# Optimization experiments

Measured on AMD Instinct MI355X. Metric: run time of the kernel, lower is better.

Reference implementation:

```python
import jax, jax.numpy as jnp
import numpy as np
import math

KAPPA = 80.0
N_REJ = 64  # fixed rounds of vectorized rejection sampling (accept prob > 0.5 per round)


def _log_iv(v, x, terms=500):
    # log of modified Bessel I_v(x) via series, in log-space for stability
    ks = np.arange(terms)
    lg1 = np.array([math.lgamma(k + 1.0) for k in range(terms)])
    lg2 = np.array([math.lgamma(v + k + 1.0) for k in range(terms)])
    logt = (v + 2.0 * ks) * np.log(x / 2.0) - lg1 - lg2
    m = logt.max()
    return m + np.log(np.exp(logt - m).sum())


def _vmf_kld(k, d):
    # matches VMF._vmf_kld: k*iv(d/2+1,k)/iv(d/2,k) + d/2*ln k - ln iv(d/2,k) - lgamma(d/2+1) - d/2*ln 2
    ratio = np.exp(_log_iv(d / 2.0 + 1.0, k) - _log_iv(d / 2.0, k))
    return (k * ratio + d / 2.0 * np.log(k) - _log_iv(d / 2.0, k)
            - math.lgamma(d / 2.0 + 1.0) - d / 2.0 * np.log(2.0))


def setup_inputs() -> dict:
    B, H, D = 16384, 1024, 512
    key = jax.random.key(0)
    k1, k2 = jax.random.split(key)
    input_repr = jax.random.normal(k1, (B, H), jnp.float32)
    W = jax.random.normal(k2, (H, D), jnp.float32) * 0.02
    b = jnp.zeros((D,), jnp.float32)
    kld = jnp.array([_vmf_kld(KAPPA, D)], jnp.float32)
    return {"input_repr": input_repr, "W": W, "b": b, "kld": kld, "n_sample": 1}


def _sample_w(key, kappa, D, batch):
    # Wood's rejection sampler for the vMF radial component, batched + masked
    dim = float(D - 1)
    bb = dim / (np.sqrt(4.0 * kappa ** 2 + dim ** 2) + 2.0 * kappa)
    xx = (1.0 - bb) / (1.0 + bb)
    cc = kappa * xx + dim * np.log(1.0 - xx ** 2)
    kz, ku = jax.random.split(key)
    z = jax.random.beta(kz, dim / 2.0, dim / 2.0, (N_REJ, batch))  # [R,B]
    u = jax.random.uniform(ku, (N_REJ, batch))
    w = (1.0 - (1.0 + bb) * z) / (1.0 - (1.0 - bb) * z)
    accept = kappa * w + dim * jnp.log(1.0 - xx * w) - cc >= jnp.log(u)
    idx = jnp.argmax(accept, axis=0)  # first accepted proposal per sample
    return w[idx, jnp.arange(batch)]  # [B]


def reference(input_repr, W, b, kld, n_sample):
    B = input_repr.shape[0]
    D = W.shape[1]
    # estimate_param: FeedForward(softplus) then L2-normalize
    mu_raw = jax.nn.softplus(input_repr @ W + b)          # [B,D]
    norm = jnp.linalg.norm(mu_raw, axis=1, keepdims=True)  # [B,1]
    redundant_norm = (norm - 1.0) ** 2                     # [B,1]
    mu = mu_raw / norm
    # sample_cell (n_sample == 1 path)
    key = jax.random.key(42)
    kw, kv = jax.random.split(key)
    w = _sample_w(kw, KAPPA, D, B)[:, None]                # [B,1]
    v = jax.random.normal(kv, (B, D), mu.dtype)
    proj = jnp.sum(mu * v, axis=1, keepdims=True)
    ortho = v - mu * proj
    v_hat = ortho / jnp.linalg.norm(ortho, axis=1, keepdims=True)
    sampled = v_hat * jnp.sqrt(1.0 - w ** 2) + mu * w      # [B,D]
    return mu, redundant_norm, kld, sampled[None]          # sampled: [1,B,D]
```

## Files before the change

kernel.cpp:

```cpp
#include <hip/hip_runtime.h>
#include <cstdint>
#include <cmath>

struct U2 { uint32_t a, b; };

__host__ __device__ inline uint32_t rotl32(uint32_t v, int r) {
    return (v << r) | (v >> (32 - r));
}

__host__ __device__ inline U2 tf2x32(U2 k, uint32_t x0, uint32_t x1) {
    uint32_t ks0 = k.a, ks1 = k.b, ks2 = k.a ^ k.b ^ 0x1BD11BDAu;
    x0 += ks0; x1 += ks1;
#define TF_R(r) { x0 += x1; x1 = rotl32(x1, r); x1 ^= x0; }
    TF_R(13) TF_R(15) TF_R(26) TF_R(6)
    x0 += ks1; x1 += ks2 + 1u;
    TF_R(17) TF_R(29) TF_R(16) TF_R(24)
    x0 += ks2; x1 += ks0 + 2u;
    TF_R(13) TF_R(15) TF_R(26) TF_R(6)
    x0 += ks0; x1 += ks1 + 3u;
    TF_R(17) TF_R(29) TF_R(16) TF_R(24)
    x0 += ks1; x1 += ks2 + 4u;
    TF_R(13) TF_R(15) TF_R(26) TF_R(6)
    x0 += ks2; x1 += ks0 + 5u;
#undef TF_R
    U2 r; r.a = x0; r.b = x1; return r;
}

__device__ inline float bits_to_u01(uint32_t bits) {
    return __uint_as_float((bits >> 9) | 0x3f800000u) - 1.0f;
}

__device__ inline float erfinv_xla(float x) {
    #pragma clang fp contract(off)
    float w = -log1pf(-(x * x));
    float p;
    if (w < 5.0f) {
        w = w - 2.5f;
        p = 2.81022636e-08f;
        p = 3.43273939e-07f + p * w;
        p = -3.5233877e-06f + p * w;
        p = -4.39150654e-06f + p * w;
        p = 0.00021858087f + p * w;
        p = -0.00125372503f + p * w;
        p = -0.00417768164f + p * w;
        p = 0.246640727f + p * w;
        p = 1.50140941f + p * w;
    } else {
        w = sqrtf(w) - 3.0f;
        p = -0.000200214257f;
        p = 0.000100950558f + p * w;
        p = 0.00134934322f + p * w;
        p = -0.00367342844f + p * w;
        p = 0.00573950773f + p * w;
        p = -0.0076224613f + p * w;
        p = 0.00943887047f + p * w;
        p = 1.00167406f + p * w;
        p = 2.83297682f + p * w;
    }
    return p * x;
}

__device__ inline float bits_to_normal(uint32_t bits) {
    #pragma clang fp contract(off)
    float f = bits_to_u01(bits);
    const float lo = -0.99999994f;
    float u = f * 2.0f + lo;
    u = fmaxf(lo, u);
    return 1.4142135623730951f * erfinv_xla(u);
}

__device__ inline float bits_to_normal_fast(uint32_t bits) {
    float f = bits_to_u01(bits);
    const float lo = -0.99999994f;
    float x = fmaxf(lo, fmaf(f, 2.0f, lo));
    float w = -__logf(fmaf(-x, x, 1.0f));
    float p;
    if (w < 5.0f) {
        w = w - 2.5f;
        p = 2.81022636e-08f;
        p = fmaf(p, w, 3.43273939e-07f);
        p = fmaf(p, w, -3.5233877e-06f);
        p = fmaf(p, w, -4.39150654e-06f);
        p = fmaf(p, w, 0.00021858087f);
        p = fmaf(p, w, -0.00125372503f);
        p = fmaf(p, w, -0.00417768164f);
        p = fmaf(p, w, 0.246640727f);
        p = fmaf(p, w, 1.50140941f);
    } else {
        w = sqrtf(w) - 3.0f;
        p = -0.000200214257f;
        p = fmaf(p, w, 0.000100950558f);
        p = fmaf(p, w, 0.00134934322f);
        p = fmaf(p, w, -0.00367342844f);
        p = fmaf(p, w, 0.00573950773f);
        p = fmaf(p, w, -0.0076224613f);
        p = fmaf(p, w, 0.00943887047f);
        p = fmaf(p, w, 1.00167406f);
        p = fmaf(p, w, 2.83297682f);
    }
    return 1.4142135623730951f * (p * x);
}

__device__ inline float normal_scalar(U2 key) {
    return bits_to_normal(tf2x32(key, 0u, 0u).a);
}

__device__ inline float uniform_scalar(U2 key) {
    uint32_t bits = tf2x32(key, 0u, 0u).a;
    return bits_to_u01(bits);
}

__device__ float gamma_log_one(U2 key, float d, float c) {
    #pragma clang fp contract(off)
    float X = 0.0f, V = 1.0f, U = 2.0f;
    for (;;) {
        float x2 = X * X;
        float sq = 1.0f - 0.0331f * (x2 * x2);
        bool cont;
        if (U < sq) {
            cont = false;
        } else {
            float rhs = X * (0.5f * X) + d * ((1.0f - V) + logf(V));
            cont = (logf(U) >= rhs);
        }
        if (!cont) break;

        U2 t03 = tf2x32(key, 0u, 3u);
        U2 t14 = tf2x32(key, 1u, 4u);
        U2 t25 = tf2x32(key, 2u, 5u);
        U2 nkey; nkey.a = t03.a; nkey.b = t14.a;
        U2 xkey; xkey.a = t25.a; xkey.b = t03.b;
        U2 Ukey; Ukey.a = t14.b; Ukey.b = t25.b;
        key = nkey;

        float x, v;
        do {
            U2 s02 = tf2x32(xkey, 0u, 2u);
            U2 s13 = tf2x32(xkey, 1u, 3u);
            U2 sub; sub.a = s02.b; sub.b = s13.b;
            xkey.a = s02.a; xkey.b = s13.a;
            x = normal_scalar(sub);
            v = 1.0f + c * x;
        } while (v <= 0.0f);
        X = x;
        V = (v * v) * v;
        U = uniform_scalar(Ukey);
    }
    return logf(d) + logf(V);
}

__device__ inline unsigned short f2bf(float f) {
    uint32_t u = __float_as_uint(f);
    uint32_t r = (u + 0x7FFFu + ((u >> 16) & 1u)) >> 16;
    return (unsigned short)r;
}

__device__ inline uint32_t pkbf2(float a, float b) {
    return (uint32_t)f2bf(a) | ((uint32_t)f2bf(b) << 16);
}

__device__ void wood_w_par(int e, U2 key_a, U2 key_b, U2 ku, float xxf,
                           float ccf, float Ap, float Bm, float d, float c,
                           float* __restrict__ w_out) {
    #pragma clang fp contract(off)
    const int lane = threadIdx.x & 63;
    const int s = lane & 3;
    const int gbase = lane & ~3;
    float w0 = 0.0f, w_sel = 0.0f;
    bool done = false;
    for (int base = 0; base < 64 && !done; base += 4) {
        const int r = base + s;
        uint32_t j = (uint32_t)r * 16384u + (uint32_t)e;
        uint32_t m0 = 2u * j, m1 = 2u * j + 1u;
        U2 ka, kb;
        if (m1 < 1048576u) {
            ka.a = tf2x32(key_a, m0, m0 + 1048576u).a;
            ka.b = tf2x32(key_a, m1, m1 + 1048576u).a;
            kb.a = tf2x32(key_b, m0, m0 + 1048576u).a;
            kb.b = tf2x32(key_b, m1, m1 + 1048576u).a;
        } else {
            ka.a = tf2x32(key_a, m0 - 1048576u, m0).b;
            ka.b = tf2x32(key_a, m1 - 1048576u, m1).b;
            kb.a = tf2x32(key_b, m0 - 1048576u, m0).b;
            kb.b = tf2x32(key_b, m1 - 1048576u, m1).b;
        }
        float lga = gamma_log_one(ka, d, c);
        float lgb = gamma_log_one(kb, d, c);
        float mx = fmaxf(lga, lgb);
        float ga = expf(lga - mx), gb = expf(lgb - mx);
        float z = ga / (ga + gb);
        uint32_t ub = (j < 524288u) ? tf2x32(ku, j, j + 524288u).a
                                    : tf2x32(ku, j - 524288u, j).b;
        float u = bits_to_u01(ub);
        float w = (1.0f - Ap * z) / (1.0f - Bm * z);
        float lhs = (80.0f * w + 511.0f * logf(1.0f - xxf * w)) - ccf;
        bool acc = lhs >= logf(u);
        if (base == 0) w0 = __shfl(w, gbase, 64);
        unsigned long long m = __ballot(acc);
        unsigned nib = (unsigned)((m >> gbase) & 0xFull);
        if (nib) {
            int first = __ffs((int)nib) - 1;
            w_sel = __shfl(w, gbase + first, 64);
            done = true;
        }
    }
    if (!done) w_sel = w0;
    if (s == 0) w_out[e] = w_sel;
}

__global__ __launch_bounds__(256) void prep3(
    const float* __restrict__ A, unsigned short* __restrict__ Ab,
    const float* __restrict__ Wm, unsigned short* __restrict__ Wt,
    const float* __restrict__ kld, float* __restrict__ kldo,
    U2 key_a, U2 key_b, U2 ku, float xxf, float ccf, float Ap, float Bm,
    float d, float c, float* __restrict__ wbuf) {
    __shared__ float t[64][65];
    const int b = blockIdx.x;
    if (b < 256) {
        const int wavid = threadIdx.x >> 6;
        const int e = b * 64 + wavid * 16 + ((threadIdx.x & 63) >> 2);
        wood_w_par(e, key_a, key_b, ku, xxf, ccf, Ap, Bm, d, c, wbuf);
    } else if (b < 4352) {
        const int row = (b - 256) * 4 + (threadIdx.x >> 6);
        const int lane = threadIdx.x & 63;
        const float* src = A + (size_t)row * 1024;
        unsigned short* dst = Ab + (size_t)row * 1024;
        const int rx = row & 7;
        #pragma unroll
        for (int q = 0; q < 4; ++q) {
            const int k0 = q * 256 + lane * 4;
            float4 v = *(const float4*)(src + k0);
            ushort4 w;
            w.x = f2bf(v.x); w.y = f2bf(v.y); w.z = f2bf(v.z); w.w = f2bf(v.w);
            const int kt = k0 >> 6;
            const int g = (k0 >> 3) & 7;
            const int e2 = k0 & 7;
            *(ushort4*)(dst + kt * 64 + ((g ^ rx) << 3) + e2) = w;
        }
    } else if (b < 4480) {
        const int tb = b - 4352;
        const int kb = tb & 15;
        const int nb = tb >> 4;
        const int tx = threadIdx.x & 63;
        const int ty = threadIdx.x >> 6;
        #pragma unroll
        for (int i = 0; i < 64; i += 4)
            t[i + ty][tx] = Wm[(size_t)(kb * 64 + i + ty) * 512 + nb * 64 + tx];
        __syncthreads();
        const int g = tx >> 3, e2 = tx & 7;
        #pragma unroll
        for (int i = 0; i < 64; i += 4) {
            int n = i + ty;
            int nglob = nb * 64 + n;
            int p = g ^ (nglob & 7);
            Wt[(size_t)nglob * 1024 + kb * 64 + p * 8 + e2] = f2bf(t[tx][n]);
        }
    } else {
        if (threadIdx.x == 0) kldo[0] = kld[0];
    }
}

typedef __attribute__((ext_vector_type(8))) short bf16x8;
typedef __attribute__((ext_vector_type(4))) float f32x4;

__device__ inline void gll16(const void* g, void* l) {
    __builtin_amdgcn_global_load_lds(
        (const __attribute__((address_space(1))) void*)g,
        (__attribute__((address_space(3))) void*)l, 16, 0, 0);
}

__global__ __launch_bounds__(256) void gemm_dma(
    const unsigned short* __restrict__ Ab, const unsigned short* __restrict__ Wt,
    const float* __restrict__ bias, float* __restrict__ out) {
    __shared__ __align__(16) unsigned short Asm[2][8192];
    __shared__ __align__(16) unsigned short Bsm[2][8192];
    const int tid = threadIdx.x;
    const int b = blockIdx.x;
    const int swz = (b & 7) * 64 + (b >> 3);
    const int bm = swz >> 2;
    const int bn = swz & 3;
    const int wave = tid >> 6, lane = tid & 63;
    const int wm = wave >> 1, wn = wave & 1;
    const int lr = lane & 15, lg = lane >> 4;

    f32x4 acc[4][4] = {};

    const char* aBase = (const char*)Ab +
        (size_t)(bm * 128 + wave * 32 + (lane >> 3)) * 2048 + (lane & 7) * 16;
    const char* bBase = (const char*)Wt +
        (size_t)(bn * 128 + wave * 32 + (lane >> 3)) * 2048 + (lane & 7) * 16;

#define STAGE(ktv, buf)                                                     \
    {                                                                       \
        _Pragma("unroll")                                                   \
        for (int ii = 0; ii < 4; ++ii) {                                    \
            const int chunk = wave * 4 + ii;                                \
            gll16(aBase + (size_t)ii * 8 * 2048 + (ktv) * 128,              \
                  (void*)&Asm[buf][chunk * 512]);                           \
            gll16(bBase + (size_t)ii * 8 * 2048 + (ktv) * 128,              \
                  (void*)&Bsm[buf][chunk * 512]);                           \
        }                                                                   \
    }

    STAGE(0, 0);
    STAGE(1, 1);
    asm volatile("s_waitcnt vmcnt(8)" ::: "memory");
    __builtin_amdgcn_s_barrier();
    __builtin_amdgcn_sched_barrier(0);

    int cur = 0;
    for (int kt = 0; kt < 16; ++kt) {
        #pragma unroll
        for (int ks = 0; ks < 2; ++ks) {
            bf16x8 af[4], bfr[4];
            #pragma unroll
            for (int mi = 0; mi < 4; ++mi) {
                const int r = wm * 64 + mi * 16 + lr;
                const int p = (ks * 4 + lg) ^ (r & 7);
                af[mi] = *(const bf16x8*)&Asm[cur][r * 64 + p * 8];
            }
            #pragma unroll
            for (int ni = 0; ni < 4; ++ni) {
                const int r = wn * 64 + ni * 16 + lr;
                const int p = (ks * 4 + lg) ^ (r & 7);
                bfr[ni] = *(const bf16x8*)&Bsm[cur][r * 64 + p * 8];
            }
            #pragma unroll
            for (int mi = 0; mi < 4; ++mi)
                #pragma unroll
                for (int ni = 0; ni < 4; ++ni)
                    acc[mi][ni] = __builtin_amdgcn_mfma_f32_16x16x32_bf16(
                        af[mi], bfr[ni], acc[mi][ni], 0, 0, 0);
        }
        __builtin_amdgcn_sched_barrier(0);
        __builtin_amdgcn_s_barrier();
        if (kt + 2 < 16) {
            STAGE(kt + 2, cur);
            asm volatile("s_waitcnt vmcnt(8)" ::: "memory");
        } else {
            asm volatile("s_waitcnt vmcnt(0)" ::: "memory");
        }
        __builtin_amdgcn_s_barrier();
        __builtin_amdgcn_sched_barrier(0);
        cur ^= 1;
    }
#undef STAGE

    #pragma unroll
    for (int mi = 0; mi < 4; ++mi) {
        #pragma unroll
        for (int ni = 0; ni < 4; ++ni) {
            const int col = bn * 128 + wn * 64 + ni * 16 + lr;
            const float bcol = bias[col];
            #pragma unroll
            for (int r = 0; r < 4; ++r) {
                const int row = bm * 128 + wm * 64 + mi * 16 + lg * 4 + r;
                float x = acc[mi][ni][r] + bcol;
                float sp = fmaxf(x, 0.0f) + __logf(1.0f + __expf(-fabsf(x)));
                out[(size_t)row * 512 + col] = sp;
            }
        }
    }
}

__device__ void wood_w_one(int i, U2 key_a, U2 key_b, U2 ku, float xxf,
                           float ccf, float Ap, float Bm, float d, float c,
                           float* __restrict__ w_out) {
    #pragma clang fp contract(off)
    float w_sel = 0.0f, w0 = 0.0f;
    bool found = false;
    for (int r = 0; r < 64 && !found; ++r) {
        uint32_t j = (uint32_t)r * 16384u + (uint32_t)i;
        uint32_t m0 = 2u * j, m1 = 2u * j + 1u;
        U2 ka, kb;
        if (m1 < 1048576u) {
            ka.a = tf2x32(key_a, m0, m0 + 1048576u).a;
            ka.b = tf2x32(key_a, m1, m1 + 1048576u).a;
            kb.a = tf2x32(key_b, m0, m0 + 1048576u).a;
            kb.b = tf2x32(key_b, m1, m1 + 1048576u).a;
        } else {
            ka.a = tf2x32(key_a, m0 - 1048576u, m0).b;
            ka.b = tf2x32(key_a, m1 - 1048576u, m1).b;
            kb.a = tf2x32(key_b, m0 - 1048576u, m0).b;
            kb.b = tf2x32(key_b, m1 - 1048576u, m1).b;
        }
        float lga = gamma_log_one(ka, d, c);
        float lgb = gamma_log_one(kb, d, c);
        float mx = fmaxf(lga, lgb);
        float ga = expf(lga - mx), gb = expf(lgb - mx);
        float z = ga / (ga + gb);
        uint32_t ub = (j < 524288u) ? tf2x32(ku, j, j + 524288u).a
                                    : tf2x32(ku, j - 524288u, j).b;
        float u = bits_to_u01(ub);
        float w = (1.0f - Ap * z) / (1.0f - Bm * z);
        float lhs = (80.0f * w + 511.0f * logf(1.0f - xxf * w)) - ccf;
        bool acc = lhs >= logf(u);
        if (r == 0) w0 = w;
        if (acc) { w_sel = w; found = true; }
    }
    w_out[i] = found ? w_sel : w0;
}

__global__ __launch_bounds__(256) void transpose_w(
    const float* __restrict__ Wm, unsigned short* __restrict__ Wt) {
    __shared__ float t[64][65];
    const int kb = blockIdx.x;
    const int nb = blockIdx.y;
    const int tx = threadIdx.x & 63;
    const int ty = threadIdx.x >> 6;
    #pragma unroll
    for (int i = 0; i < 64; i += 4)
        t[i + ty][tx] = Wm[(size_t)(kb * 64 + i + ty) * 512 + nb * 64 + tx];
    __syncthreads();
    const int g = tx >> 3, e = tx & 7;
    #pragma unroll
    for (int i = 0; i < 64; i += 4) {
        int n = i + ty;
        int nglob = nb * 64 + n;
        int p = g ^ (nglob & 7);
        Wt[(size_t)nglob * 1024 + kb * 64 + p * 8 + e] = f2bf(t[tx][n]);
    }
}

__global__ __launch_bounds__(256) void gemm_bf16(
    const float* __restrict__ A, const unsigned short* __restrict__ Wt,
    const float* __restrict__ bias, float* __restrict__ out) {
    __shared__ __align__(16) unsigned short Asm[128 * 64];
    __shared__ __align__(16) unsigned short Bsm[128 * 64];
    const int tid = threadIdx.x;
    const int b = blockIdx.x;
    const int swz = (b & 7) * 64 + (b >> 3);
    const int bm = swz >> 2;
    const int bn = swz & 3;
    const int wave = tid >> 6, lane = tid & 63;
    const int wm = wave >> 1, wn = wave & 1;
    const int lr = lane & 15, lg = lane >> 4;

    f32x4 acc[4][4] = {};

    const int ar = tid >> 1;
    const int ah = tid & 1;
    const float* Ap = A + (size_t)(bm * 128 + ar) * 1024 + ah * 32;
    const int arx = ar & 7;

    const char* WtB = (const char*)Wt;
    const int brow = bn * 128 + (wave * 4) * 8 + (lane >> 3);
    const int bposb = (lane & 7) * 16;

    for (int kt = 0; kt < 16; ++kt) {
        #pragma unroll
        for (int ii = 0; ii < 4; ++ii) {
            const int chunk = wave * 4 + ii;
            const void* src = WtB + (size_t)(brow + ii * 8) * 2048 + kt * 128 + bposb;
            gll16(src, (void*)&Bsm[chunk * 512]);
        }
        const float* srcA = Ap + kt * 64;
        #pragma unroll
        for (int st = 0; st < 4; ++st) {
            float4 y0 = *(const float4*)(srcA + st * 8);
            float4 y1 = *(const float4*)(srcA + st * 8 + 4);
            uint4 uv;
            uv.x = pkbf2(y0.x, y0.y);
            uv.y = pkbf2(y0.z, y0.w);
            uv.z = pkbf2(y1.x, y1.y);
            uv.w = pkbf2(y1.z, y1.w);
            const int gblk = ah * 4 + st;
            const int p = gblk ^ arx;
            *(uint4*)&Asm[ar * 64 + p * 8] = uv;
        }
        __syncthreads();

        #pragma unroll
        for (int ks = 0; ks < 2; ++ks) {
            bf16x8 af[4], bfr[4];
            #pragma unroll
            for (int mi = 0; mi < 4; ++mi) {
                const int r = wm * 64 + mi * 16 + lr;
                const int p = (ks * 4 + lg) ^ (r & 7);
                af[mi] = *(const bf16x8*)&Asm[r * 64 + p * 8];
            }
            #pragma unroll
            for (int ni = 0; ni < 4; ++ni) {
                const int r = wn * 64 + ni * 16 + lr;
                const int p = (ks * 4 + lg) ^ (r & 7);
                bfr[ni] = *(const bf16x8*)&Bsm[r * 64 + p * 8];
            }
            #pragma unroll
            for (int mi = 0; mi < 4; ++mi)
                #pragma unroll
                for (int ni = 0; ni < 4; ++ni)
                    acc[mi][ni] = __builtin_amdgcn_mfma_f32_16x16x32_bf16(
                        af[mi], bfr[ni], acc[mi][ni], 0, 0, 0);
        }
        __syncthreads();
    }

    #pragma unroll
    for (int mi = 0; mi < 4; ++mi) {
        #pragma unroll
        for (int ni = 0; ni < 4; ++ni) {
            const int col = bn * 128 + wn * 64 + ni * 16 + lr;
            const float bcol = bias[col];
            #pragma unroll
            for (int r = 0; r < 4; ++r) {
                const int row = bm * 128 + wm * 64 + mi * 16 + lg * 4 + r;
                float x = acc[mi][ni][r] + bcol;
                float sp = fmaxf(x, 0.0f) + log1pf(expf(-fabsf(x)));
                out[(size_t)row * 512 + col] = sp;
            }
        }
    }
}

__global__ __launch_bounds__(64) void compute_w_kernel(
    U2 key_a, U2 key_b, U2 ku, float xxf, float ccf, float Ap, float Bm,
    float d, float c, float* __restrict__ w_out) {
    const int i = blockIdx.x * blockDim.x + threadIdx.x;
    if (i >= 16384) return;
    wood_w_one(i, key_a, key_b, ku, xxf, ccf, Ap, Bm, d, c, w_out);
}

__global__ void copy_kld(const float* __restrict__ kld, float* __restrict__ dst) {
    if (blockIdx.x == 0 && threadIdx.x == 0) dst[0] = kld[0];
}

__device__ inline float wave_allreduce(float s) {
    #pragma unroll
    for (int off = 1; off < 64; off <<= 1) s += __shfl_xor(s, off);
    return s;
}

__global__ __launch_bounds__(256) void finalize2(
    const float* muraw, float* muout, float* __restrict__ rn,
    const float* __restrict__ wv, U2 kv, float* smp) {
    const int p = blockIdx.x * 4 + (threadIdx.x >> 6);
    const int lane = threadIdx.x & 63;
    const int r0 = p, r1 = p + 8192;
    const float* q0 = muraw + (size_t)r0 * 512;
    const float* q1 = muraw + (size_t)r1 * 512;

    float m0[8], m1[8];
    {
        float4 t0 = *(const float4*)(q0 + lane * 4);
        float4 t1 = *(const float4*)(q0 + 256 + lane * 4);
        m0[0] = t0.x; m0[1] = t0.y; m0[2] = t0.z; m0[3] = t0.w;
        m0[4] = t1.x; m0[5] = t1.y; m0[6] = t1.z; m0[7] = t1.w;
        float4 t2 = *(const float4*)(q1 + lane * 4);
        float4 t3 = *(const float4*)(q1 + 256 + lane * 4);
        m1[0] = t2.x; m1[1] = t2.y; m1[2] = t2.z; m1[3] = t2.w;
        m1[4] = t3.x; m1[5] = t3.y; m1[6] = t3.z; m1[7] = t3.w;
    }

    float ss0 = 0.0f, ss1 = 0.0f;
    #pragma unroll
    for (int j = 0; j < 8; ++j) { ss0 += m0[j] * m0[j]; ss1 += m1[j] * m1[j]; }
    float n0 = sqrtf(wave_allreduce(ss0));
    float n1 = sqrtf(wave_allreduce(ss1));
    if (lane == 0) {
        float d0 = n0 - 1.0f, d1 = n1 - 1.0f;
        rn[r0] = d0 * d0;
        rn[r1] = d1 * d1;
    }
    float in0 = 1.0f / n0, in1 = 1.0f / n1;
    #pragma unroll
    for (int j = 0; j < 8; ++j) { m0[j] *= in0; m1[j] *= in1; }

    float v0[8], v1[8];
    #pragma unroll
    for (int j = 0; j < 8; ++j) {
        const int c = (j < 4) ? (lane * 4 + j) : (256 + lane * 4 + (j - 4));
        uint32_t idx = (uint32_t)p * 512u + (uint32_t)c;
        U2 h = tf2x32(kv, idx, idx + 4194304u);
        v0[j] = bits_to_normal_fast(h.a);
        v1[j] = bits_to_normal_fast(h.b);
    }

    float p0 = 0.0f, p1 = 0.0f;
    #pragma unroll
    for (int j = 0; j < 8; ++j) { p0 += m0[j] * v0[j]; p1 += m1[j] * v1[j]; }
    p0 = wave_allreduce(p0);
    p1 = wave_allreduce(p1);

    float o0[8], o1[8];
    float s0 = 0.0f, s1 = 0.0f;
    #pragma unroll
    for (int j = 0; j < 8; ++j) {
        o0[j] = v0[j] - m0[j] * p0; s0 += o0[j] * o0[j];
        o1[j] = v1[j] - m1[j] * p1; s1 += o1[j] * o1[j];
    }
    float f0, f1, w0, w1;
    {
        float on0 = sqrtf(wave_allreduce(s0));
        float on1 = sqrtf(wave_allreduce(s1));
        w0 = wv[r0]; w1 = wv[r1];
        f0 = sqrtf(1.0f - w0 * w0) / on0;
        f1 = sqrtf(1.0f - w1 * w1) / on1;
    }

    float* pm0 = muout + (size_t)r0 * 512;
    float* pm1 = muout + (size_t)r1 * 512;
    float* op0 = smp + (size_t)r0 * 512;
    float* op1 = smp + (size_t)r1 * 512;
    float4 wvec;
    wvec.x = o0[0] * f0 + m0[0] * w0; wvec.y = o0[1] * f0 + m0[1] * w0;
    wvec.z = o0[2] * f0 + m0[2] * w0; wvec.w = o0[3] * f0 + m0[3] * w0;
    *(float4*)(op0 + lane * 4) = wvec;
    wvec.x = o0[4] * f0 + m0[4] * w0; wvec.y = o0[5] * f0 + m0[5] * w0;
    wvec.z = o0[6] * f0 + m0[6] * w0; wvec.w = o0[7] * f0 + m0[7] * w0;
    *(float4*)(op0 + 256 + lane * 4) = wvec;
    wvec.x = o1[0] * f1 + m1[0] * w1; wvec.y = o1[1] * f1 + m1[1] * w1;
    wvec.z = o1[2] * f1 + m1[2] * w1; wvec.w = o1[3] * f1 + m1[3] * w1;
    *(float4*)(op1 + lane * 4) = wvec;
    wvec.x = o1[4] * f1 + m1[4] * w1; wvec.y = o1[5] * f1 + m1[5] * w1;
    wvec.z = o1[6] * f1 + m1[6] * w1; wvec.w = o1[7] * f1 + m1[7] * w1;
    *(float4*)(op1 + 256 + lane * 4) = wvec;

    wvec.x = m0[0]; wvec.y = m0[1]; wvec.z = m0[2]; wvec.w = m0[3];
    *(float4*)(pm0 + lane * 4) = wvec;
    wvec.x = m0[4]; wvec.y = m0[5]; wvec.z = m0[6]; wvec.w = m0[7];
    *(float4*)(pm0 + 256 + lane * 4) = wvec;
    wvec.x = m1[0]; wvec.y = m1[1]; wvec.z = m1[2]; wvec.w = m1[3];
    *(float4*)(pm1 + lane * 4) = wvec;
    wvec.x = m1[4]; wvec.y = m1[5]; wvec.z = m1[6]; wvec.w = m1[7];
    *(float4*)(pm1 + 256 + lane * 4) = wvec;
}

extern "C" void kernel_launch(void* const* d_in, const int* in_sizes, int n_in,
                              void* d_out, int out_size, void* d_ws, size_t ws_size,
                              hipStream_t stream) {
    const float* A    = (const float*)d_in[0];
    const float* Wm   = (const float*)d_in[1];
    const float* bias = (const float*)d_in[2];
    const float* kld  = (const float*)d_in[3];

    float* out = (float*)d_out;
    float* mu   = out;
    float* rn   = out + 8388608;
    float* kldo = out + 8388608 + 16384;
    float* smp  = kldo + 1;
    float* wbuf = (float*)d_ws;

    U2 root; root.a = 0u; root.b = 42u;
    U2 t02 = tf2x32(root, 0u, 2u), t13 = tf2x32(root, 1u, 3u);
    U2 kw; kw.a = t02.a; kw.b = t13.a;
    U2 kv; kv.a = t02.b; kv.b = t13.b;
    U2 s02 = tf2x32(kw, 0u, 2u), s13 = tf2x32(kw, 1u, 3u);
    U2 kz; kz.a = s02.a; kz.b = s13.a;
    U2 ku; ku.a = s02.b; ku.b = s13.b;
    U2 b02 = tf2x32(kz, 0u, 2u), b13 = tf2x32(kz, 1u, 3u);
    U2 key_a; key_a.a = b02.a; key_a.b = b13.a;
    U2 key_b; key_b.a = b02.b; key_b.b = b13.b;

    const double kappa = 80.0, dim = 511.0;
    double bb = dim / (sqrt(4.0 * kappa * kappa + dim * dim) + 2.0 * kappa);
    double xxd = (1.0 - bb) / (1.0 + bb);
    double ccd = kappa * xxd + dim * log(1.0 - xxd * xxd);
    float xxf = (float)xxd, ccf = (float)ccd;
    float Apc = (float)(1.0 + bb), Bmc = (float)(1.0 - bb);
    float one3 = 1.0f / 3.0f;
    float dml = 255.5f - one3;
    float cml = one3 / sqrtf(dml);

    const bool bigws = ws_size >= (size_t)(65536 + 1048576);
    if (bigws) {
        unsigned short* Ab = (unsigned short*)d_out;
        unsigned short* Wt = (unsigned short*)((char*)d_ws + 65536);
        float* muraw = smp;
        prep3<<<4481, 256, 0, stream>>>(A, Ab, Wm, Wt, kld, kldo,
                                        key_a, key_b, ku, xxf, ccf, Apc, Bmc,
                                        dml, cml, wbuf);
        gemm_dma<<<512, 256, 0, stream>>>(Ab, Wt, bias, muraw);
        finalize2<<<2048, 256, 0, stream>>>(muraw, mu, rn, wbuf, kv, smp);
    } else {
        unsigned short* Wt = (unsigned short*)((char*)d_out + 33619984);
        compute_w_kernel<<<256, 64, 0, stream>>>(key_a, key_b, ku, xxf, ccf,
                                                 Apc, Bmc, dml, cml, wbuf);
        transpose_w<<<dim3(16, 8), 256, 0, stream>>>(Wm, Wt);
        gemm_bf16<<<512, 256, 0, stream>>>(A, Wt, bias, mu);
        finalize2<<<2048, 256, 0, stream>>>(mu, mu, rn, wbuf, kv, smp);
        copy_kld<<<1, 64, 0, stream>>>(kld, kldo);
    }
}
```

Before: 69.75 us.

## Fuse GEMM with normalize and vMF sampling epilogue in one kernel

Replaces the 128x128-tile GEMM plus separate finalize kernel with a single kernel where each 512-thread block computes full 512-column rows for 32 rows (two 16-row groups), then does softplus, L2 norm, random normal generation, projection and sampling in the epilogue using cross-wave shared-memory reductions. The bf16 staging layout changes to 32-wide K tiles with a 4-way swizzle. This removes the round trip of the raw mu matrix through global memory and one kernel launch. In exchange, the A-operand tile is small, so the whole W matrix is re-read from L2 by every block, and the epilogue adds several block barriers.

```diff
diff --git a/kernel.cpp b/kernel.cpp
--- a/kernel.cpp
+++ b/kernel.cpp
@@ -208,7 +208,7 @@
     if (s == 0) w_out[e] = w_sel;
 }
 
-__global__ __launch_bounds__(256) void prep3(
+__global__ __launch_bounds__(256) void prep4(
     const float* __restrict__ A, unsigned short* __restrict__ Ab,
     const float* __restrict__ Wm, unsigned short* __restrict__ Wt,
     const float* __restrict__ kld, float* __restrict__ kldo,
@@ -225,17 +225,17 @@
         const int lane = threadIdx.x & 63;
         const float* src = A + (size_t)row * 1024;
         unsigned short* dst = Ab + (size_t)row * 1024;
-        const int rx = row & 7;
+        const int rx = (row >> 1) & 3;
         #pragma unroll
         for (int q = 0; q < 4; ++q) {
             const int k0 = q * 256 + lane * 4;
             float4 v = *(const float4*)(src + k0);
             ushort4 w;
             w.x = f2bf(v.x); w.y = f2bf(v.y); w.z = f2bf(v.z); w.w = f2bf(v.w);
-            const int kt = k0 >> 6;
-            const int g = (k0 >> 3) & 7;
+            const int kt = k0 >> 5;
+            const int g = (k0 >> 3) & 3;
             const int e2 = k0 & 7;
-            *(ushort4*)(dst + kt * 64 + ((g ^ rx) << 3) + e2) = w;
+            *(ushort4*)(dst + kt * 32 + ((g ^ rx) << 3) + e2) = w;
         }
     } else if (b < 4480) {
         const int tb = b - 4352;
@@ -247,13 +247,15 @@
         for (int i = 0; i < 64; i += 4)
             t[i + ty][tx] = Wm[(size_t)(kb * 64 + i + ty) * 512 + nb * 64 + tx];
         __syncthreads();
-        const int g = tx >> 3, e2 = tx & 7;
+        const int kt = (tx >> 5);
+        const int g = (tx >> 3) & 3;
+        const int e2 = tx & 7;
         #pragma unroll
         for (int i = 0; i < 64; i += 4) {
             int n = i + ty;
             int nglob = nb * 64 + n;
-            int p = g ^ (nglob & 7);
-            Wt[(size_t)nglob * 1024 + kb * 64 + p * 8 + e2] = f2bf(t[tx][n]);
+            int p = g ^ ((nglob >> 1) & 3);
+            Wt[(size_t)nglob * 1024 + (kb * 2 + kt) * 32 + p * 8 + e2] = f2bf(t[tx][n]);
         }
     } else {
         if (threadIdx.x == 0) kldo[0] = kld[0];
@@ -269,74 +271,80 @@
         (__attribute__((address_space(3))) void*)l, 16, 0, 0);
 }
 
-__global__ __launch_bounds__(256) void gemm_dma(
-    const unsigned short* __restrict__ Ab, const unsigned short* __restrict__ Wt,
-    const float* __restrict__ bias, float* __restrict__ out) {
-    __shared__ __align__(16) unsigned short Asm[2][8192];
-    __shared__ __align__(16) unsigned short Bsm[2][8192];
+__global__ __launch_bounds__(512, 2) void gemm_fin(
+    const unsigned short* Ab, const unsigned short* __restrict__ Wt,
+    const float* __restrict__ bias, const float* __restrict__ wv, U2 kv,
+    float* mu, float* __restrict__ rn, float* __restrict__ smp) {
+    __shared__ __align__(16) unsigned short AsT[2][32 * 32];
+    __shared__ __align__(16) unsigned short BsT[2][512 * 32];
+    __shared__ float partA[8][32], partB[8][32], partC[8][32];
+    __shared__ float totA[32], totB[32], totC[32];
+
     const int tid = threadIdx.x;
     const int b = blockIdx.x;
-    const int swz = (b & 7) * 64 + (b >> 3);
-    const int bm = swz >> 2;
-    const int bn = swz & 3;
-    const int wave = tid >> 6, lane = tid & 63;
-    const int wm = wave >> 1, wn = wave & 1;
+    const int w = tid >> 6;
+    const int lane = tid & 63;
     const int lr = lane & 15, lg = lane >> 4;
-
-    f32x4 acc[4][4] = {};
-
-    const char* aBase = (const char*)Ab +
-        (size_t)(bm * 128 + wave * 32 + (lane >> 3)) * 2048 + (lane & 7) * 16;
-    const char* bBase = (const char*)Wt +
-        (size_t)(bn * 128 + wave * 32 + (lane >> 3)) * 2048 + (lane & 7) * 16;
-
-#define STAGE(ktv, buf)                                                     \
-    {                                                                       \
-        _Pragma("unroll")                                                   \
-        for (int ii = 0; ii < 4; ++ii) {                                    \
-            const int chunk = wave * 4 + ii;                                \
-            gll16(aBase + (size_t)ii * 8 * 2048 + (ktv) * 128,              \
-                  (void*)&Asm[buf][chunk * 512]);                           \
-            gll16(bBase + (size_t)ii * 8 * 2048 + (ktv) * 128,              \
-                  (void*)&Bsm[buf][chunk * 512]);                           \
-        }                                                                   \
-    }
-
-    STAGE(0, 0);
-    STAGE(1, 1);
-    asm volatile("s_waitcnt vmcnt(8)" ::: "memory");
+    const int rlo0 = b * 16;
+    const int rhi0 = 8192 + b * 16;
+
+    const char* AbB = (const char*)Ab;
+    const char* WtB = (const char*)Wt;
+
+    f32x4 acc[2][4] = {};
+
+#define STAGEF(ktv, buf)                                                     \
+    {                                                                        \
+        _Pragma("unroll")                                                    \
+        for (int ii = 0; ii < 4; ++ii) {                                     \
+            const int s = w * 256 + ii * 64 + lane;                          \
+            gll16(WtB + (size_t)(s >> 2) * 2048 + (ktv) * 64 + (s & 3) * 16, \
+                  (void*)&BsT[buf][(size_t)(w * 256 + ii * 64) * 8]);        \
+        }                                                                    \
+        {                                                                    \
+            const int sa = w * 16 + lane;                                    \
+            const int m = sa >> 2, p = sa & 3;                               \
+            const size_t row = (m < 16) ? (size_t)(rlo0 + m)                 \
+                                        : (size_t)(rhi0 + m - 16);           \
+            if (lane < 16)                                                   \
+                gll16(AbB + row * 2048 + (ktv) * 64 + p * 16,                \
+                      (void*)&AsT[buf][(size_t)(w * 16) * 8]);               \
+        }                                                                    \
+    }
+
+    STAGEF(0, 0);
+    STAGEF(1, 1);
+    asm volatile("s_waitcnt vmcnt(5)" ::: "memory");
     __builtin_amdgcn_s_barrier();
     __builtin_amdgcn_sched_barrier(0);
 
     int cur = 0;
-    for (int kt = 0; kt < 16; ++kt) {
-        #pragma unroll
-        for (int ks = 0; ks < 2; ++ks) {
-            bf16x8 af[4], bfr[4];
-            #pragma unroll
-            for (int mi = 0; mi < 4; ++mi) {
-                const int r = wm * 64 + mi * 16 + lr;
-                const int p = (ks * 4 + lg) ^ (r & 7);
-                af[mi] = *(const bf16x8*)&Asm[cur][r * 64 + p * 8];
-            }
-            #pragma unroll
-            for (int ni = 0; ni < 4; ++ni) {
-                const int r = wn * 64 + ni * 16 + lr;
-                const int p = (ks * 4 + lg) ^ (r & 7);
-                bfr[ni] = *(const bf16x8*)&Bsm[cur][r * 64 + p * 8];
-            }
-            #pragma unroll
-            for (int mi = 0; mi < 4; ++mi)
-                #pragma unroll
-                for (int ni = 0; ni < 4; ++ni)
-                    acc[mi][ni] = __builtin_amdgcn_mfma_f32_16x16x32_bf16(
-                        af[mi], bfr[ni], acc[mi][ni], 0, 0, 0);
-        }
+    for (int kt = 0; kt < 32; ++kt) {
+        bf16x8 af[2], bfr[4];
+        #pragma unroll
+        for (int fr = 0; fr < 2; ++fr) {
+            const int m = fr * 16 + lr;
+            const int p = lg ^ ((m >> 1) & 3);
+            af[fr] = *(const bf16x8*)&AsT[cur][m * 32 + p * 8];
+        }
+        #pragma unroll
+        for (int fc = 0; fc < 4; ++fc) {
+            const int n = w * 64 + fc * 16 + lr;
+            const int p = lg ^ ((n >> 1) & 3);
+            bfr[fc] = *(const bf16x8*)&BsT[cur][n * 32 + p * 8];
+        }
+        #pragma unroll
+        for (int fr = 0; fr < 2; ++fr)
+            #pragma unroll
+            for (int fc = 0; fc < 4; ++fc)
+                acc[fr][fc] = __builtin_amdgcn_mfma_f32_16x16x32_bf16(
+                    af[fr], bfr[fc], acc[fr][fc], 0, 0, 0);
+
         __builtin_amdgcn_sched_barrier(0);
         __builtin_amdgcn_s_barrier();
-        if (kt + 2 < 16) {
-            STAGE(kt + 2, cur);
-            asm volatile("s_waitcnt vmcnt(8)" ::: "memory");
+        if (kt + 2 < 32) {
+            STAGEF(kt + 2, cur);
+            asm volatile("s_waitcnt vmcnt(5)" ::: "memory");
         } else {
             asm volatile("s_waitcnt vmcnt(0)" ::: "memory");
         }
@@ -344,23 +352,201 @@
         __builtin_amdgcn_sched_barrier(0);
         cur ^= 1;
     }
-#undef STAGE
-
-    #pragma unroll
-    for (int mi = 0; mi < 4; ++mi) {
-        #pragma unroll
-        for (int ni = 0; ni < 4; ++ni) {
-            const int col = bn * 128 + wn * 64 + ni * 16 + lr;
-            const float bcol = bias[col];
-            #pragma unroll
-            for (int r = 0; r < 4; ++r) {
-                const int row = bm * 128 + wm * 64 + mi * 16 + lg * 4 + r;
-                float x = acc[mi][ni][r] + bcol;
-                float sp = fmaxf(x, 0.0f) + __logf(1.0f + __expf(-fabsf(x)));
-                out[(size_t)row * 512 + col] = sp;
+#undef STAGEF
+
+    float bv[4];
+    #pragma unroll
+    for (int fc = 0; fc < 4; ++fc) bv[fc] = bias[w * 64 + fc * 16 + lr];
+    #pragma unroll
+    for (int fr = 0; fr < 2; ++fr)
+        #pragma unroll
+        for (int fc = 0; fc < 4; ++fc)
+            #pragma unroll
+            for (int j = 0; j < 4; ++j) {
+                float x = acc[fr][fc][j] + bv[fc];
+                acc[fr][fc][j] = fmaxf(x, 0.0f) + __logf(1.0f + __expf(-fabsf(x)));
             }
-        }
-    }
+
+    {
+        float pt[2][4];
+        #pragma unroll
+        for (int fr = 0; fr < 2; ++fr)
+            #pragma unroll
+            for (int j = 0; j < 4; ++j) {
+                float s = 0.0f;
+                #pragma unroll
+                for (int fc = 0; fc < 4; ++fc) s += acc[fr][fc][j] * acc[fr][fc][j];
+                pt[fr][j] = s;
+            }
+        #pragma unroll
+        for (int off = 8; off > 0; off >>= 1)
+            #pragma unroll
+            for (int fr = 0; fr < 2; ++fr)
+                #pragma unroll
+                for (int j = 0; j < 4; ++j)
+                    pt[fr][j] += __shfl_xor(pt[fr][j], off);
+        if (lr == 0) {
+            #pragma unroll
+            for (int fr = 0; fr < 2; ++fr)
+                #pragma unroll
+                for (int j = 0; j < 4; ++j)
+                    partA[w][fr * 16 + lg * 4 + j] = pt[fr][j];
+        }
+    }
+    __syncthreads();
+    if (w == 0 && lane < 32) {
+        float s = 0.0f;
+        #pragma unroll
+        for (int ww = 0; ww < 8; ++ww) s += partA[ww][lane];
+        totA[lane] = s;
+    }
+    __syncthreads();
+
+    float inv[2][4], nrm[2][4];
+    #pragma unroll
+    for (int fr = 0; fr < 2; ++fr)
+        #pragma unroll
+        for (int j = 0; j < 4; ++j) {
+            nrm[fr][j] = sqrtf(totA[fr * 16 + lg * 4 + j]);
+            inv[fr][j] = 1.0f / nrm[fr][j];
+        }
+    if (w == 0 && lr == 0) {
+        #pragma unroll
+        for (int fr = 0; fr < 2; ++fr)
+            #pragma unroll
+            for (int j = 0; j < 4; ++j) {
+                int row = (fr ? rhi0 : rlo0) + lg * 4 + j;
+                float dm = nrm[fr][j] - 1.0f;
+                rn[row] = dm * dm;
+            }
+    }
+    #pragma unroll
+    for (int fr = 0; fr < 2; ++fr)
+        #pragma unroll
+        for (int fc = 0; fc < 4; ++fc)
+            #pragma unroll
+            for (int j = 0; j < 4; ++j)
+                acc[fr][fc][j] *= inv[fr][j];
+
+    float v0[4][4], v1[4][4];
+    #pragma unroll
+    for (int j = 0; j < 4; ++j)
+        #pragma unroll
+        for (int fc = 0; fc < 4; ++fc) {
+            uint32_t idx = (uint32_t)(rlo0 + lg * 4 + j) * 512u
+                         + (uint32_t)(w * 64 + fc * 16 + lr);
+            U2 h = tf2x32(kv, idx, idx + 4194304u);
+            v0[j][fc] = bits_to_normal_fast(h.a);
+            v1[j][fc] = bits_to_normal_fast(h.b);
+        }
+
+    {
+        float pt[2][4];
+        #pragma unroll
+        for (int j = 0; j < 4; ++j) {
+            float s0 = 0.0f, s1 = 0.0f;
+            #pragma unroll
+            for (int fc = 0; fc < 4; ++fc) {
+                s0 += acc[0][fc][j] * v0[j][fc];
+                s1 += acc[1][fc][j] * v1[j][fc];
+            }
+            pt[0][j] = s0; pt[1][j] = s1;
+        }
+        #pragma unroll
+        for (int off = 8; off > 0; off >>= 1)
+            #pragma unroll
+            for (int fr = 0; fr < 2; ++fr)
+                #pragma unroll
+                for (int j = 0; j < 4; ++j)
+                    pt[fr][j] += __shfl_xor(pt[fr][j], off);
+        if (lr == 0) {
+            #pragma unroll
+            for (int fr = 0; fr < 2; ++fr)
+                #pragma unroll
+                for (int j = 0; j < 4; ++j)
+                    partB[w][fr * 16 + lg * 4 + j] = pt[fr][j];
+        }
+    }
+    __syncthreads();
+    if (w == 0 && lane < 32) {
+        float s = 0.0f;
+        #pragma unroll
+        for (int ww = 0; ww < 8; ++ww) s += partB[ww][lane];
+        totB[lane] = s;
+    }
+    __syncthreads();
+
+    float proj[2][4];
+    #pragma unroll
+    for (int fr = 0; fr < 2; ++fr)
+        #pragma unroll
+        for (int j = 0; j < 4; ++j)
+            proj[fr][j] = totB[fr * 16 + lg * 4 + j];
+
+    {
+        float pt[2][4];
+        #pragma unroll
+        for (int j = 0; j < 4; ++j) {
+            float s0 = 0.0f, s1 = 0.0f;
+            #pragma unroll
+            for (int fc = 0; fc < 4; ++fc) {
+                v0[j][fc] -= acc[0][fc][j] * proj[0][j];
+                v1[j][fc] -= acc[1][fc][j] * proj[1][j];
+                s0 += v0[j][fc] * v0[j][fc];
+                s1 += v1[j][fc] * v1[j][fc];
+            }
+            pt[0][j] = s0; pt[1][j] = s1;
+        }
+        #pragma unroll
+        for (int off = 8; off > 0; off >>= 1)
+            #pragma unroll
+            for (int fr = 0; fr < 2; ++fr)
+                #pragma unroll
+                for (int j = 0; j < 4; ++j)
+                    pt[fr][j] += __shfl_xor(pt[fr][j], off);
+        if (lr == 0) {
+            #pragma unroll
+            for (int fr = 0; fr < 2; ++fr)
+                #pragma unroll
+                for (int j = 0; j < 4; ++j)
+                    partC[w][fr * 16 + lg * 4 + j] = pt[fr][j];
+        }
+    }
+    __syncthreads();
+    if (w == 0 && lane < 32) {
+        float s = 0.0f;
+        #pragma unroll
+        for (int ww = 0; ww < 8; ++ww) s += partC[ww][lane];
+        totC[lane] = s;
+    }
+    __syncthreads();
+
+    float ff[2][4], wval[2][4];
+    #pragma unroll
+    for (int fr = 0; fr < 2; ++fr)
+        #pragma unroll
+        for (int j = 0; j < 4; ++j) {
+            int row = (fr ? rhi0 : rlo0) + lg * 4 + j;
+            float wr = wv[row];
+            wval[fr][j] = wr;
+            float onorm = sqrtf(totC[fr * 16 + lg * 4 + j]);
+            ff[fr][j] = sqrtf(1.0f - wr * wr) / onorm;
+        }
+
+    #pragma unroll
+    for (int fr = 0; fr < 2; ++fr)
+        #pragma unroll
+        for (int fc = 0; fc < 4; ++fc) {
+            const int col = w * 64 + fc * 16 + lr;
+            #pragma unroll
+            for (int j = 0; j < 4; ++j) {
+                const int row = (fr ? rhi0 : rlo0) + lg * 4 + j;
+                float muv = acc[fr][fc][j];
+                float ov = fr ? v1[j][fc] : v0[j][fc];
+                smp[(size_t)row * 512 + col] = ov * ff[fr][j] + muv * wval[fr][j];
+                mu[(size_t)row * 512 + col] = muv;
+            }
+        }
 }
 
 __device__ void wood_w_one(int i, U2 key_a, U2 key_b, U2 ku, float xxf,
@@ -665,12 +851,10 @@
     if (bigws) {
         unsigned short* Ab = (unsigned short*)d_out;
         unsigned short* Wt = (unsigned short*)((char*)d_ws + 65536);
-        float* muraw = smp;
-        prep3<<<4481, 256, 0, stream>>>(A, Ab, Wm, Wt, kld, kldo,
+        prep4<<<4481, 256, 0, stream>>>(A, Ab, Wm, Wt, kld, kldo,
                                         key_a, key_b, ku, xxf, ccf, Apc, Bmc,
                                         dml, cml, wbuf);
-        gemm_dma<<<512, 256, 0, stream>>>(Ab, Wt, bias, muraw);
-        finalize2<<<2048, 256, 0, stream>>>(muraw, mu, rn, wbuf, kv, smp);
+        gemm_fin<<<512, 512, 0, stream>>>(Ab, Wt, bias, wbuf, kv, mu, rn, smp);
     } else {
         unsigned short* Wt = (unsigned short*)((char*)d_out + 33619984);
         compute_w_kernel<<<256, 64, 0, stream>>>(key_a, key_b, ku, xxf, ccf,
```

New measurement: 90.75 us. 1.3x slower.

## Load A operand directly to registers instead of staging through LDS

Applied to the files above, without the earlier changes.

The GEMM now fetches A-tile fragments straight from global memory into VGPR double buffers with inline global_load_dwordx4, and only B goes through LDS via global_load_lds. The prep kernel stops swizzling A and writes bf16 rows linearly. The aim is to halve LDS traffic and LDS reads per MFMA step. The cost is higher register pressure from two 8-entry u32x4 banks and uncoalesced 16-byte row-strided global reads of A, each of which is duplicated across the two waves sharing a row band.

```diff
diff --git a/kernel.cpp b/kernel.cpp
--- a/kernel.cpp
+++ b/kernel.cpp
@@ -225,17 +225,13 @@
         const int lane = threadIdx.x & 63;
         const float* src = A + (size_t)row * 1024;
         unsigned short* dst = Ab + (size_t)row * 1024;
-        const int rx = row & 7;
         #pragma unroll
         for (int q = 0; q < 4; ++q) {
             const int k0 = q * 256 + lane * 4;
             float4 v = *(const float4*)(src + k0);
             ushort4 w;
             w.x = f2bf(v.x); w.y = f2bf(v.y); w.z = f2bf(v.z); w.w = f2bf(v.w);
-            const int kt = k0 >> 6;
-            const int g = (k0 >> 3) & 7;
-            const int e2 = k0 & 7;
-            *(ushort4*)(dst + kt * 64 + ((g ^ rx) << 3) + e2) = w;
+            *(ushort4*)(dst + k0) = w;
         }
     } else if (b < 4480) {
         const int tb = b - 4352;
@@ -262,6 +258,7 @@
 
 typedef __attribute__((ext_vector_type(8))) short bf16x8;
 typedef __attribute__((ext_vector_type(4))) float f32x4;
+typedef __attribute__((ext_vector_type(4))) unsigned int u32x4;
 
 __device__ inline void gll16(const void* g, void* l) {
     __builtin_amdgcn_global_load_lds(
@@ -269,10 +266,9 @@
         (__attribute__((address_space(3))) void*)l, 16, 0, 0);
 }
 
-__global__ __launch_bounds__(256) void gemm_dma(
+__global__ __launch_bounds__(256) void gemm_rdma(
     const unsigned short* __restrict__ Ab, const unsigned short* __restrict__ Wt,
     const float* __restrict__ bias, float* __restrict__ out) {
-    __shared__ __align__(16) unsigned short Asm[2][8192];
     __shared__ __align__(16) unsigned short Bsm[2][8192];
     const int tid = threadIdx.x;
     const int b = blockIdx.x;
@@ -284,67 +280,87 @@
     const int lr = lane & 15, lg = lane >> 4;
 
     f32x4 acc[4][4] = {};
-
-    const char* aBase = (const char*)Ab +
-        (size_t)(bm * 128 + wave * 32 + (lane >> 3)) * 2048 + (lane & 7) * 16;
+    u32x4 a0[8], a1[8];
+
+    const char* aptr[4];
+    #pragma unroll
+    for (int mi = 0; mi < 4; ++mi)
+        aptr[mi] = (const char*)Ab +
+            (size_t)(bm * 128 + wm * 64 + mi * 16 + lr) * 2048 + lg * 16;
+
     const char* bBase = (const char*)Wt +
         (size_t)(bn * 128 + wave * 32 + (lane >> 3)) * 2048 + (lane & 7) * 16;
 
-#define STAGE(ktv, buf)                                                     \
+#define LOADA(bank, ktv)                                                    \
+    {                                                                       \
+        _Pragma("unroll")                                                   \
+        for (int mi = 0; mi < 4; ++mi)                                      \
+            _Pragma("unroll")                                               \
+            for (int ks = 0; ks < 2; ++ks)                                  \
+                asm volatile("global_load_dwordx4 %0, %1, off"              \
+                             : "=v"(bank[mi * 2 + ks])                      \
+                             : "v"(aptr[mi] + (ktv) * 128 + ks * 64));      \
+    }
+
+#define STAGEB(ktv, buf)                                                    \
     {                                                                       \
         _Pragma("unroll")                                                   \
         for (int ii = 0; ii < 4; ++ii) {                                    \
             const int chunk = wave * 4 + ii;                                \
-            gll16(aBase + (size_t)ii * 8 * 2048 + (ktv) * 128,              \
-                  (void*)&Asm[buf][chunk * 512]);                           \
             gll16(bBase + (size_t)ii * 8 * 2048 + (ktv) * 128,              \
                   (void*)&Bsm[buf][chunk * 512]);                           \
         }                                                                   \
     }
 
-    STAGE(0, 0);
-    STAGE(1, 1);
-    asm volatile("s_waitcnt vmcnt(8)" ::: "memory");
+#define BODY(bank, buf, ktv)                                                \
+    {                                                                       \
+        _Pragma("unroll")                                                   \
+        for (int ks = 0; ks < 2; ++ks) {                                    \
+            bf16x8 bfr[4];                                                  \
+            _Pragma("unroll")                                               \
+            for (int ni = 0; ni < 4; ++ni) {                                \
+                const int r = wn * 64 + ni * 16 + lr;                       \
+                const int p = (ks * 4 + lg) ^ (r & 7);                      \
+                bfr[ni] = *(const bf16x8*)&Bsm[buf][r * 64 + p * 8];        \
+            }                                                               \
+            _Pragma("unroll")                                               \
+            for (int mi = 0; mi < 4; ++mi) {                                \
+                bf16x8 afv = __builtin_bit_cast(bf16x8, bank[mi * 2 + ks]); \
+                _Pragma("unroll")                                           \
+                for (int ni = 0; ni < 4; ++ni)                              \
+                    acc[mi][ni] = __builtin_amdgcn_mfma_f32_16x16x32_bf16(  \
+                        afv, bfr[ni], acc[mi][ni], 0, 0, 0);                \
+            }                                                               \
+        }                                                                   \
+        __builtin_amdgcn_sched_barrier(0);                                  \
+        __builtin_amdgcn_s_barrier();                                       \
+        if ((ktv) + 2 < 16) {                                               \
+            LOADA(bank, (ktv) + 2);                                         \
+            STAGEB((ktv) + 2, buf);                                         \
+            asm volatile("s_waitcnt vmcnt(12)" ::: "memory");               \
+        } else {                                                            \
+            asm volatile("s_waitcnt vmcnt(0)" ::: "memory");                \
+        }                                                                   \
+        __builtin_amdgcn_s_barrier();                                       \
+        __builtin_amdgcn_sched_barrier(0);                                  \
+    }
+
+    LOADA(a0, 0);
+    STAGEB(0, 0);
+    __builtin_amdgcn_sched_barrier(0);
+    LOADA(a1, 1);
+    STAGEB(1, 1);
+    asm volatile("s_waitcnt vmcnt(12)" ::: "memory");
     __builtin_amdgcn_s_barrier();
     __builtin_amdgcn_sched_barrier(0);
 
-    int cur = 0;
-    for (int kt = 0; kt < 16; ++kt) {
-        #pragma unroll
-        for (int ks = 0; ks < 2; ++ks) {
-            bf16x8 af[4], bfr[4];
-            #pragma unroll
-            for (int mi = 0; mi < 4; ++mi) {
-                const int r = wm * 64 + mi * 16 + lr;
-                const int p = (ks * 4 + lg) ^ (r & 7);
-                af[mi] = *(const bf16x8*)&Asm[cur][r * 64 + p * 8];
-            }
-            #pragma unroll
-            for (int ni = 0; ni < 4; ++ni) {
-                const int r = wn * 64 + ni * 16 + lr;
-                const int p = (ks * 4 + lg) ^ (r & 7);
-                bfr[ni] = *(const bf16x8*)&Bsm[cur][r * 64 + p * 8];
-            }
-            #pragma unroll
-            for (int mi = 0; mi < 4; ++mi)
-                #pragma unroll
-                for (int ni = 0; ni < 4; ++ni)
-                    acc[mi][ni] = __builtin_amdgcn_mfma_f32_16x16x32_bf16(
-                        af[mi], bfr[ni], acc[mi][ni], 0, 0, 0);
-        }
-        __builtin_amdgcn_sched_barrier(0);
-        __builtin_amdgcn_s_barrier();
-        if (kt + 2 < 16) {
-            STAGE(kt + 2, cur);
-            asm volatile("s_waitcnt vmcnt(8)" ::: "memory");
-        } else {
-            asm volatile("s_waitcnt vmcnt(0)" ::: "memory");
-        }
-        __builtin_amdgcn_s_barrier();
-        __builtin_amdgcn_sched_barrier(0);
-        cur ^= 1;
-    }
-#undef STAGE
+    for (int ktt = 0; ktt < 16; ktt += 2) {
+        BODY(a0, 0, ktt);
+        BODY(a1, 1, ktt + 1);
+    }
+#undef BODY
+#undef STAGEB
+#undef LOADA
 
     #pragma unroll
     for (int mi = 0; mi < 4; ++mi) {
@@ -669,7 +685,7 @@
         prep3<<<4481, 256, 0, stream>>>(A, Ab, Wm, Wt, kld, kldo,
                                         key_a, key_b, ku, xxf, ccf, Apc, Bmc,
                                         dml, cml, wbuf);
-        gemm_dma<<<512, 256, 0, stream>>>(Ab, Wt, bias, muraw);
+        gemm_rdma<<<512, 256, 0, stream>>>(Ab, Wt, bias, muraw);
         finalize2<<<2048, 256, 0, stream>>>(muraw, mu, rn, wbuf, kv, smp);
     } else {
         unsigned short* Wt = (unsigned short*)((char*)d_out + 33619984);
```

Result: slower. 83.20 us (+19.3%).
